# Kernel tuning notes

Measured on AMD Instinct MI355X. Metric: run time of the kernel, lower is better.

The kernel has to match this reference:

```python
import jax, jax.numpy as jnp
import numpy as np

EMB_DIM = 1024
HEAD_NUM = 16
HEAD_DIM = EMB_DIM // HEAD_NUM
B, S = 2, 2048


def setup_inputs() -> dict:
    key = jax.random.key(0)
    k_x, k_wqkv, k_bqkv, k_wo, k_bo = jax.random.split(key, 5)
    x = jax.random.normal(k_x, (B, S, EMB_DIM), dtype=jnp.float32)
    # nn.Linear default init scale ~ 1/sqrt(fan_in); exact distribution irrelevant for a reference
    lim = 1.0 / np.sqrt(EMB_DIM)
    W_qkv = jax.random.uniform(k_wqkv, (EMB_DIM, 3 * EMB_DIM), jnp.float32, -lim, lim)
    b_qkv = jax.random.uniform(k_bqkv, (3 * EMB_DIM,), jnp.float32, -lim, lim)
    W_o = jax.random.uniform(k_wo, (EMB_DIM, EMB_DIM), jnp.float32, -lim, lim)
    b_o = jax.random.uniform(k_bo, (EMB_DIM,), jnp.float32, -lim, lim)
    mask = jnp.tril(jnp.ones((S, S), dtype=bool))  # causal mask as in casual_mask(seq_len)
    return {"x": x, "W_qkv": W_qkv, "b_qkv": b_qkv, "W_o": W_o, "b_o": b_o, "mask": mask}


def reference(x, W_qkv, b_qkv, W_o, b_o, mask):
    b, s, e = x.shape
    qkv = x @ W_qkv + b_qkv                      # [b, s, 3e]
    q, k, v = qkv[..., :e], qkv[..., e:2 * e], qkv[..., 2 * e:]
    # [b, s, h, d] -> [b, h, s, d]
    q = q.reshape(b, s, HEAD_NUM, HEAD_DIM).transpose(0, 2, 1, 3)
    k = k.reshape(b, s, HEAD_NUM, HEAD_DIM).transpose(0, 2, 1, 3)
    v = v.reshape(b, s, HEAD_NUM, HEAD_DIM).transpose(0, 2, 1, 3)
    scores = jnp.einsum("bhqd,bhkd->bhqk", q, k) / jnp.sqrt(jnp.float32(HEAD_DIM))
    scores = jnp.where(mask, scores, -jnp.inf)   # masked_fill(~mask, -inf)
    probs = jax.nn.softmax(scores, axis=-1)      # dropout is identity in eval mode
    out = jnp.einsum("bhqk,bhkd->bhqd", probs, v)
    out = out.transpose(0, 2, 1, 3).reshape(b, s, e)
    return out @ W_o + b_o
```

## Files before the change

### kernel.cpp

```cpp
#include <hip/hip_runtime.h>


typedef __attribute__((ext_vector_type(8))) short short8;
typedef __attribute__((ext_vector_type(4))) short short4v;
typedef __attribute__((ext_vector_type(4))) float floatx4;

#define NB 2
#define SEQ 2048
#define EMB 1024
#define NH 16
#define HD 64
#define M_ROWS (NB * SEQ)
#define N_QKV (3 * EMB)
#define SLOT_B 8448

#define GLL(g, l) __builtin_amdgcn_global_load_lds( \
    (const __attribute__((address_space(1))) void*)(g), \
    (__attribute__((address_space(3))) void*)(l), 16, 0, 0)

#if defined(__HIP_DEVICE_COMPILE__)
#define MFMA16K16(A, B, C) __builtin_amdgcn_mfma_f32_16x16x16bf16_1k(A, B, C, 0, 0, 0)
#else
#define MFMA16K16(A, B, C) (C)
#endif

static __device__ __forceinline__ unsigned short f2bf(float f) {
    union { float f; unsigned int u; } v; v.f = f;
    unsigned int r = v.u + 0x7FFFu + ((v.u >> 16) & 1u);
    return (unsigned short)(r >> 16);
}
static __device__ __forceinline__ float bf2f(unsigned short h) {
    union { unsigned int u; float f; } v; v.u = ((unsigned int)h) << 16;
    return v.f;
}

__global__ void prep(const float* __restrict__ x,
                     const float* __restrict__ Wqkv, const float* __restrict__ Wo,
                     unsigned short* __restrict__ x_bf,
                     unsigned short* __restrict__ wqkvT, unsigned short* __restrict__ woT) {
    __shared__ unsigned short tile[32][33];
    int z = blockIdx.z;
    int tx = threadIdx.x, ty = threadIdx.y;
    if (z == 2) {
        int id = ((int)blockIdx.y * 96 + (int)blockIdx.x) * 256 + ty * 32 + tx;
        const int n4 = M_ROWS * EMB / 4;
        for (int i = id; i < n4; i += 96 * 32 * 256) {
            float4 v = ((const float4*)x)[i];
            unsigned long long p = (unsigned long long)f2bf(v.x)
                | ((unsigned long long)f2bf(v.y) << 16)
                | ((unsigned long long)f2bf(v.z) << 32)
                | ((unsigned long long)f2bf(v.w) << 48);
            ((unsigned long long*)x_bf)[i] = p;
        }
        return;
    }
    int C = z ? EMB : N_QKV;
    if ((int)blockIdx.x * 32 >= C) return;
    const float* in = z ? Wo : Wqkv;
    unsigned short* out = z ? woT : wqkvT;
    const int R = EMB;
    int c0 = blockIdx.x * 32, r0 = blockIdx.y * 32;
    #pragma unroll
    for (int j = 0; j < 4; ++j)
        tile[ty + j * 8][tx] = f2bf(in[(size_t)(r0 + ty + j * 8) * C + c0 + tx]);
    __syncthreads();
    #pragma unroll
    for (int j = 0; j < 4; ++j)
        out[(size_t)(c0 + ty + j * 8) * R + r0 + tx] = tile[tx][ty + j * 8];
}

#define CTS 130

__global__ __launch_bounds__(256) void qkv_gemm(
    const unsigned short* __restrict__ A,
    const unsigned short* __restrict__ Bt,
    const float* __restrict__ bias,
    unsigned short* __restrict__ qb, unsigned short* __restrict__ kb,
    unsigned short* __restrict__ vb)
{
    const int K = EMB;
    __shared__ __align__(16) unsigned short smem[128 * CTS];

    int t = threadIdx.x;
    int m0 = blockIdx.y * 128;
    int n0 = blockIdx.x * 128;
    int w = t >> 6, lane = t & 63, quad = lane >> 4, lcol = lane & 15;
    int wr = w >> 1, wc = w & 1;

    floatx4 zero = {0.f, 0.f, 0.f, 0.f};
    floatx4 acc[4][4];
    #pragma unroll
    for (int i = 0; i < 4; ++i)
        #pragma unroll
        for (int j = 0; j < 4; ++j) acc[i][j] = zero;

    const unsigned short* a0 = A  + (size_t)(m0 + (t >> 2)) * K + ((t & 3) << 3);
    const unsigned short* b0 = Bt + (size_t)(n0 + (t >> 2)) * K + ((t & 3) << 3);
    unsigned short* la = &smem[t << 3];

    GLL(a0, la);
    GLL(a0 + 64 * K, la + 2048);
    GLL(b0, la + 4096);
    GLL(b0 + 64 * K, la + 6144);

    for (int k0 = 0; k0 < K; k0 += 32) {
        int cur = (k0 >> 5) & 1, nxt = cur ^ 1;
        __syncthreads();
        if (k0 + 32 < K) {
            GLL(a0 + k0 + 32, la + nxt * 8192);
            GLL(a0 + 64 * K + k0 + 32, la + nxt * 8192 + 2048);
            GLL(b0 + k0 + 32, la + nxt * 8192 + 4096);
            GLL(b0 + 64 * K + k0 + 32, la + nxt * 8192 + 6144);
        }
        const unsigned short* As = &smem[cur * 8192];
        const unsigned short* Bs = As + 4096;
        short8 af[4], bfm[4];
        #pragma unroll
        for (int i = 0; i < 4; ++i)
            af[i] = *(const short8*)(&As[(wr * 64 + i * 16 + lcol) * 32 + quad * 8]);
        #pragma unroll
        for (int j = 0; j < 4; ++j)
            bfm[j] = *(const short8*)(&Bs[(wc * 64 + j * 16 + lcol) * 32 + quad * 8]);
        #pragma unroll
        for (int i = 0; i < 4; ++i)
            #pragma unroll
            for (int j = 0; j < 4; ++j)
                acc[i][j] = __builtin_amdgcn_mfma_f32_16x16x32_bf16(af[i], bfm[j], acc[i][j], 0, 0, 0);
    }

    bool isV = (n0 >= 2 * EMB);
    __syncthreads();
    #pragma unroll
    for (int i = 0; i < 4; ++i) {
        int row0 = wr * 64 + i * 16 + quad * 4;
        #pragma unroll
        for (int j = 0; j < 4; ++j) {
            int col = wc * 64 + j * 16 + lcol;
            float bv = bias[n0 + col];
            #pragma unroll
            for (int r = 0; r < 4; ++r) {
                unsigned short hv = f2bf(acc[i][j][r] + bv);
                if (isV) smem[col * CTS + row0 + r] = hv;
                else     smem[(row0 + r) * CTS + col] = hv;
            }
        }
    }
    __syncthreads();

    int b = m0 >> 11, s0 = m0 & 2047;
    int hbase = (n0 & 1023) >> 6;
    if (!isV) {
        unsigned short* dst = (n0 >= EMB) ? kb : qb;
        #pragma unroll
        for (int it = 0; it < 8; ++it) {
            int job = it * 32 + (t >> 3);
            int tok = job & 127, hh = job >> 7;
            int chunk = t & 7;
            short8 vv = *(const short8*)(&smem[tok * CTS + hh * 64 + chunk * 8]);
            size_t g = ((size_t)((b * NH + hbase + hh) * SEQ + s0 + tok)) * HD + chunk * 8;
            *(short8*)(&dst[g]) = vv;
        }
    } else {
        #pragma unroll
        for (int it = 0; it < 8; ++it) {
            int job = it * 32 + (t >> 3);
            int f = job & 127, half = job >> 7;
            int chunk = (t & 7) + half * 8;
            short8 vv = *(const short8*)(&smem[f * CTS + chunk * 8]);
            int h = hbase + (f >> 6), d = f & 63;
            size_t g = ((size_t)((b * NH + h) * HD + d)) * SEQ + s0 + chunk * 8;
            *(short8*)(&vb[g]) = vv;
        }
    }
}

__global__ __launch_bounds__(256) void attn_partial(
    const unsigned short* __restrict__ Q,
    const unsigned short* __restrict__ Kk,
    const unsigned short* __restrict__ Vt,
    unsigned short* __restrict__ Out,
    unsigned char* __restrict__ Part)
{
    __shared__ __align__(16) unsigned short Ks[2][64 * 64];
    __shared__ __align__(16) unsigned short Vs[2][64 * 64];

    int u = blockIdx.x;
    int bh = blockIdx.y;
    int qt, c;
    if (u < 16) { qt = u; c = 0; }
    else { int v = u - 16; qt = 16 + (v >> 1); c = v & 1; }
    int ktBeg = c << 4;
    int ktEnd = (c == 0 && qt >= 16) ? 16 : (qt + 1);

    int q0 = qt * 64;
    int t = threadIdx.x;
    int w = t >> 6, lane = t & 63, quad = lane >> 4, lcol = lane & 15;
    const size_t hoff = (size_t)bh * SEQ * HD;
    const float SC = 0.18033688011112043f;

    const unsigned short* qp = Q + hoff + (size_t)(q0 + 16 * w + lcol) * HD + quad * 8;
    short8 aq0 = *(const short8*)qp, aq1 = *(const short8*)(qp + 32);

    int srow = t >> 3;
    int ss   = (t & 7) ^ (srow & 7);
    const unsigned short* kgl = Kk + hoff + (size_t)srow * HD + ss * 8;
    const unsigned short* vgl = Vt + hoff + (size_t)srow * SEQ + ss * 8;
    unsigned short* kld = &Ks[0][t * 8];
    unsigned short* vld = &Vs[0][t * 8];

    floatx4 zero = {0.f, 0.f, 0.f, 0.f};
    floatx4 O[4];
    floatx4 lacc = zero;
    #pragma unroll
    for (int d = 0; d < 4; ++d) O[d] = zero;

    short4v ones4;
    #pragma unroll
    for (int j = 0; j < 4; ++j) ones4[j] = (short)0x3F80;

    {
        int k0 = ktBeg * 64;
        GLL(kgl + (size_t)k0 * HD, kld);
        GLL(kgl + (size_t)(k0 + 32) * HD, kld + 2048);
        GLL(vgl + k0, vld);
        GLL(vgl + (size_t)32 * SEQ + k0, vld + 2048);
    }

    int sx0 = (quad ^ (lcol & 7)) << 3;
    int sx1 = sx0 ^ 32;

    for (int kt = ktBeg; kt < ktEnd; ++kt) {
        int cur = kt & 1, nxt = cur ^ 1;
        __syncthreads();
        if (kt + 1 < ktEnd) {
            int k0 = (kt + 1) * 64;
            GLL(kgl + (size_t)k0 * HD, kld + nxt * 4096);
            GLL(kgl + (size_t)(k0 + 32) * HD, kld + nxt * 4096 + 2048);
            GLL(vgl + k0, vld + nxt * 4096);
            GLL(vgl + (size_t)32 * SEQ + k0, vld + nxt * 4096 + 2048);
        }

        const unsigned short* ksr = &Ks[cur][0];
        const unsigned short* vsr = &Vs[cur][0];
        short8 bk0[4], bk1[4];
        #pragma unroll
        for (int tc = 0; tc < 4; ++tc) {
            int rb = (tc * 16 + lcol) << 6;
            bk0[tc] = *(const short8*)(ksr + rb + sx0);
            bk1[tc] = *(const short8*)(ksr + rb + sx1);
        }

        floatx4 sacc[4];
        #pragma unroll
        for (int tc = 0; tc < 4; ++tc) {
            sacc[tc] = __builtin_amdgcn_mfma_f32_16x16x32_bf16(bk0[tc], aq0, zero, 0, 0, 0);
            sacc[tc] = __builtin_amdgcn_mfma_f32_16x16x32_bf16(bk1[tc], aq1, sacc[tc], 0, 0, 0);
        }

        short4v pk[4];
        if (kt == qt) {
            int qrow = q0 + 16 * w + lcol;
            int kbase = kt * 64 + quad * 4;
            #pragma unroll
            for (int tc = 0; tc < 4; ++tc) {
                #pragma unroll
                for (int r = 0; r < 4; ++r) {
                    float p = __builtin_amdgcn_exp2f(sacc[tc][r] * SC);
                    if (kbase + tc * 16 + r > qrow) p = 0.f;
                    pk[tc][r] = (short)f2bf(p);
                }
            }
        } else {
            #pragma unroll
            for (int tc = 0; tc < 4; ++tc) {
                #pragma unroll
                for (int r = 0; r < 4; ++r)
                    pk[tc][r] = (short)f2bf(__builtin_amdgcn_exp2f(sacc[tc][r] * SC));
            }
        }

        #pragma unroll
        for (int td = 0; td < 4; ++td) {
            short4v va[4];
            #pragma unroll
            for (int tc = 0; tc < 4; ++tc) {
                int seg = ((tc << 1) + (quad >> 1)) ^ (lcol & 7);
                va[tc] = *(const short4v*)(vsr + ((td * 16 + lcol) << 6) + (seg << 3) + ((quad & 1) << 2));
            }
            #pragma unroll
            for (int tc = 0; tc < 4; ++tc)
                O[td] = MFMA16K16(va[tc], pk[tc], O[td]);
        }
        #pragma unroll
        for (int tc = 0; tc < 4; ++tc)
            lacc = MFMA16K16(ones4, pk[tc], lacc);
    }

    int qrow = q0 + 16 * w + lcol;
    if (qt < 16) {
        int b = bh >> 4, h = bh & 15;
        float inv = 1.0f / lacc[0];
        size_t obase = ((size_t)b * SEQ + qrow) * EMB + (size_t)h * HD + quad * 4;
        #pragma unroll
        for (int td = 0; td < 4; ++td) {
            short4v ov;
            #pragma unroll
            for (int r = 0; r < 4; ++r) ov[r] = (short)f2bf(O[td][r] * inv);
            *(short4v*)(&Out[obase + td * 16]) = ov;
        }
    } else {
        unsigned char* sp = Part + ((size_t)(bh * 16 + (qt - 16)) * 2 + c) * SLOT_B;
        unsigned short* sO = (unsigned short*)sp;
        float* sL = (float*)(sp + 8192);
        int ql = 16 * w + lcol;
        #pragma unroll
        for (int td = 0; td < 4; ++td) {
            short4v ov;
            #pragma unroll
            for (int r = 0; r < 4; ++r) ov[r] = (short)f2bf(O[td][r]);
            *(short4v*)(&sO[ql * 64 + td * 16 + quad * 4]) = ov;
        }
        if (quad == 0) sL[ql] = lacc[0];
    }
}

__global__ __launch_bounds__(256) void attn_combine(
    const unsigned char* __restrict__ Part, unsigned short* __restrict__ Out)
{
    int qh = blockIdx.x;
    int bh = blockIdx.y;
    int qt = 16 + qh;
    const unsigned char* s0 = Part + ((size_t)(bh * 16 + qh) * 2) * SLOT_B;
    const unsigned char* s1 = s0 + SLOT_B;
    const unsigned short* O0 = (const unsigned short*)s0;
    const unsigned short* O1 = (const unsigned short*)s1;
    const float* L0 = (const float*)(s0 + 8192);
    const float* L1 = (const float*)(s1 + 8192);
    int b = bh >> 4, h = bh & 15;
    size_t obase = ((size_t)b * SEQ + qt * 64) * EMB + (size_t)h * HD;
    int t = threadIdx.x;
    #pragma unroll
    for (int it = 0; it < 16; ++it) {
        int idx = it * 256 + t;
        int row = idx >> 6, col = idx & 63;
        float lv = L0[row] + L1[row];
        float v = (bf2f(O0[idx]) + bf2f(O1[idx])) / lv;
        Out[obase + (size_t)row * EMB + col] = f2bf(v);
    }
}

__global__ __launch_bounds__(256) void oproj_gemm(
    const unsigned short* __restrict__ A,
    const unsigned short* __restrict__ Bt,
    const float* __restrict__ bias,
    float* __restrict__ Cout)
{
    const int K = EMB;
    __shared__ __align__(16) unsigned short smem[2 * 8192];
    int t = threadIdx.x;
    int m0 = blockIdx.y * 128;
    int n0 = blockIdx.x * 128;
    int w = t >> 6, lane = t & 63, quad = lane >> 4, lcol = lane & 15;
    int wr = w >> 1, wc = w & 1;

    floatx4 zero = {0.f, 0.f, 0.f, 0.f};
    floatx4 acc[4][4];
    #pragma unroll
    for (int i = 0; i < 4; ++i)
        #pragma unroll
        for (int j = 0; j < 4; ++j) acc[i][j] = zero;

    const unsigned short* a0 = A  + (size_t)(m0 + (t >> 2)) * K + ((t & 3) << 3);
    const unsigned short* b0 = Bt + (size_t)(n0 + (t >> 2)) * K + ((t & 3) << 3);
    unsigned short* la = &smem[t << 3];

    GLL(a0, la);
    GLL(a0 + 64 * K, la + 2048);
    GLL(b0, la + 4096);
    GLL(b0 + 64 * K, la + 6144);

    for (int k0 = 0; k0 < K; k0 += 32) {
        int cur = (k0 >> 5) & 1, nxt = cur ^ 1;
        __syncthreads();
        if (k0 + 32 < K) {
            GLL(a0 + k0 + 32, la + nxt * 8192);
            GLL(a0 + 64 * K + k0 + 32, la + nxt * 8192 + 2048);
            GLL(b0 + k0 + 32, la + nxt * 8192 + 4096);
            GLL(b0 + 64 * K + k0 + 32, la + nxt * 8192 + 6144);
        }
        const unsigned short* As = &smem[cur * 8192];
        const unsigned short* Bs = As + 4096;
        short8 af[4], bfm[4];
        #pragma unroll
        for (int i = 0; i < 4; ++i)
            af[i] = *(const short8*)(&As[(wr * 64 + i * 16 + lcol) * 32 + quad * 8]);
        #pragma unroll
        for (int j = 0; j < 4; ++j)
            bfm[j] = *(const short8*)(&Bs[(wc * 64 + j * 16 + lcol) * 32 + quad * 8]);
        #pragma unroll
        for (int i = 0; i < 4; ++i)
            #pragma unroll
            for (int j = 0; j < 4; ++j)
                acc[i][j] = __builtin_amdgcn_mfma_f32_16x16x32_bf16(af[i], bfm[j], acc[i][j], 0, 0, 0);
    }

    #pragma unroll
    for (int i = 0; i < 4; ++i) {
        int m = m0 + wr * 64 + i * 16 + quad * 4;
        #pragma unroll
        for (int j = 0; j < 4; ++j) {
            int n = n0 + wc * 64 + j * 16 + lcol;
            float bv = bias[n];
            #pragma unroll
            for (int r = 0; r < 4; ++r)
                Cout[(size_t)(m + r) * EMB + n] = acc[i][j][r] + bv;
        }
    }
}

extern "C" void kernel_launch(void* const* d_in, const int* in_sizes, int n_in,
                              void* d_out, int out_size, void* d_ws, size_t ws_size,
                              hipStream_t stream) {
    (void)in_sizes; (void)n_in; (void)out_size; (void)ws_size;
    char* ws = (char*)d_ws;
    const size_t OFF_X     = 0;
    const size_t OFF_WQKVT = OFF_X     + (size_t)M_ROWS * EMB * 2;
    const size_t OFF_WOT   = OFF_WQKVT + (size_t)N_QKV * EMB * 2;
    const size_t OFF_Q     = OFF_WOT   + (size_t)EMB * EMB * 2;
    const size_t OFF_K     = OFF_Q     + (size_t)M_ROWS * EMB * 2;
    const size_t OFF_V     = OFF_K     + (size_t)M_ROWS * EMB * 2;
    const size_t OFF_ATTN  = OFF_V     + (size_t)M_ROWS * EMB * 2;
    const size_t OFF_PART  = OFF_ATTN  + (size_t)M_ROWS * EMB * 2;

    const float* x    = (const float*)d_in[0];
    const float* Wqkv = (const float*)d_in[1];
    const float* bqkv = (const float*)d_in[2];
    const float* Wo   = (const float*)d_in[3];
    const float* bo   = (const float*)d_in[4];

    unsigned short* x_bf  = (unsigned short*)(ws + OFF_X);
    unsigned short* wqkvT = (unsigned short*)(ws + OFF_WQKVT);
    unsigned short* woT   = (unsigned short*)(ws + OFF_WOT);
    unsigned short* qb    = (unsigned short*)(ws + OFF_Q);
    unsigned short* kb    = (unsigned short*)(ws + OFF_K);
    unsigned short* vb    = (unsigned short*)(ws + OFF_V);
    unsigned short* attn  = (unsigned short*)(ws + OFF_ATTN);
    unsigned char*  part  = (unsigned char*)(ws + OFF_PART);

    prep<<<dim3(96, 32, 3), dim3(32, 8), 0, stream>>>(x, Wqkv, Wo, x_bf, wqkvT, woT);

    qkv_gemm<<<dim3(N_QKV / 128, M_ROWS / 128), 256, 0, stream>>>(x_bf, wqkvT, bqkv, qb, kb, vb);
    attn_partial<<<dim3(48, NB * NH), 256, 0, stream>>>(qb, kb, vb, attn, part);
    attn_combine<<<dim3(16, NB * NH), 256, 0, stream>>>(part, attn);
    oproj_gemm<<<dim3(EMB / 128, M_ROWS / 128), 256, 0, stream>>>(attn, woT, bo, (float*)d_out);
}
```

Baseline: 199.5 us.

## Fuse split-K attention combine into partial kernel via atomic last-arriver

The separate attn_combine launch is removed. The last of the two split blocks, detected by an atomic counter whose flags are zeroed in prep, now merges the partial outputs in place. The softmax scale is folded into Q in the QKV GEMM epilogue. V fragments are loaded before the MFMA loop, and bf16 packing uses a byte-permute truncation instead of round-to-nearest. This saves a kernel launch and some per-element multiplies, at the cost of threadfences and atomics, more register pressure, and slightly different rounding.

```diff
diff --git a/kernel.cpp b/kernel.cpp
--- a/kernel.cpp
+++ b/kernel.cpp
@@ -13,6 +13,7 @@
 #define M_ROWS (NB * SEQ)
 #define N_QKV (3 * EMB)
 #define SLOT_B 8448
+#define SC_Q 0.18033688011112043f
 
 #define GLL(g, l) __builtin_amdgcn_global_load_lds( \
     (const __attribute__((address_space(1))) void*)(g), \
@@ -33,11 +34,16 @@
     union { unsigned int u; float f; } v; v.u = ((unsigned int)h) << 16;
     return v.f;
 }
+static __device__ __forceinline__ unsigned int pkhi(float a, float b) {
+    union { float f; unsigned int u; } ua, ub; ua.f = a; ub.f = b;
+    return __builtin_amdgcn_perm(ub.u, ua.u, 0x07060302u);
+}
 
 __global__ void prep(const float* __restrict__ x,
                      const float* __restrict__ Wqkv, const float* __restrict__ Wo,
                      unsigned short* __restrict__ x_bf,
-                     unsigned short* __restrict__ wqkvT, unsigned short* __restrict__ woT) {
+                     unsigned short* __restrict__ wqkvT, unsigned short* __restrict__ woT,
+                     int* __restrict__ flags) {
     __shared__ unsigned short tile[32][33];
     int z = blockIdx.z;
     int tx = threadIdx.x, ty = threadIdx.y;
@@ -56,6 +62,11 @@
     }
     int C = z ? EMB : N_QKV;
     if ((int)blockIdx.x * 32 >= C) return;
+    if (z == 1 && blockIdx.x == 0 && blockIdx.y == 0) {
+        int id = ty * 32 + tx;
+        flags[id] = 0;
+        flags[id + 256] = 0;
+    }
     const float* in = z ? Wo : Wqkv;
     unsigned short* out = z ? woT : wqkvT;
     const int R = EMB;
@@ -129,6 +140,7 @@
     }
 
     bool isV = (n0 >= 2 * EMB);
+    float scl = (n0 < EMB) ? SC_Q : 1.0f;
     __syncthreads();
     #pragma unroll
     for (int i = 0; i < 4; ++i) {
@@ -139,7 +151,7 @@
             float bv = bias[n0 + col];
             #pragma unroll
             for (int r = 0; r < 4; ++r) {
-                unsigned short hv = f2bf(acc[i][j][r] + bv);
+                unsigned short hv = f2bf((acc[i][j][r] + bv) * scl);
                 if (isV) smem[col * CTS + row0 + r] = hv;
                 else     smem[(row0 + r) * CTS + col] = hv;
             }
@@ -179,10 +191,12 @@
     const unsigned short* __restrict__ Kk,
     const unsigned short* __restrict__ Vt,
     unsigned short* __restrict__ Out,
-    unsigned char* __restrict__ Part)
+    unsigned char* __restrict__ Part,
+    int* __restrict__ Flag)
 {
     __shared__ __align__(16) unsigned short Ks[2][64 * 64];
     __shared__ __align__(16) unsigned short Vs[2][64 * 64];
+    __shared__ int sArr;
 
     int u = blockIdx.x;
     int bh = blockIdx.y;
@@ -196,7 +210,6 @@
     int t = threadIdx.x;
     int w = t >> 6, lane = t & 63, quad = lane >> 4, lcol = lane & 15;
     const size_t hoff = (size_t)bh * SEQ * HD;
-    const float SC = 0.18033688011112043f;
 
     const unsigned short* qp = Q + hoff + (size_t)(q0 + 16 * w + lcol) * HD + quad * 8;
     short8 aq0 = *(const short8*)qp, aq1 = *(const short8*)(qp + 32);
@@ -228,6 +241,7 @@
 
     int sx0 = (quad ^ (lcol & 7)) << 3;
     int sx1 = sx0 ^ 32;
+    int qrow = q0 + 16 * w + lcol;
 
     for (int kt = ktBeg; kt < ktEnd; ++kt) {
         int cur = kt & 1, nxt = cur ^ 1;
@@ -249,6 +263,14 @@
             bk0[tc] = *(const short8*)(ksr + rb + sx0);
             bk1[tc] = *(const short8*)(ksr + rb + sx1);
         }
+        short4v vaf[4][4];
+        #pragma unroll
+        for (int td = 0; td < 4; ++td)
+            #pragma unroll
+            for (int tc = 0; tc < 4; ++tc) {
+                int seg = ((tc << 1) + (quad >> 1)) ^ (lcol & 7);
+                vaf[td][tc] = *(const short4v*)(vsr + ((td * 16 + lcol) << 6) + (seg << 3) + ((quad & 1) << 2));
+            }
 
         floatx4 sacc[4];
         #pragma unroll
@@ -257,95 +279,83 @@
             sacc[tc] = __builtin_amdgcn_mfma_f32_16x16x32_bf16(bk1[tc], aq1, sacc[tc], 0, 0, 0);
         }
 
+        bool diag = (kt == qt);
         short4v pk[4];
-        if (kt == qt) {
-            int qrow = q0 + 16 * w + lcol;
-            int kbase = kt * 64 + quad * 4;
-            #pragma unroll
-            for (int tc = 0; tc < 4; ++tc) {
-                #pragma unroll
-                for (int r = 0; r < 4; ++r) {
-                    float p = __builtin_amdgcn_exp2f(sacc[tc][r] * SC);
-                    if (kbase + tc * 16 + r > qrow) p = 0.f;
-                    pk[tc][r] = (short)f2bf(p);
-                }
-            }
-        } else {
-            #pragma unroll
-            for (int tc = 0; tc < 4; ++tc) {
+        #pragma unroll
+        for (int tc = 0; tc < 4; ++tc) {
+            float pv[4];
+            #pragma unroll
+            for (int r = 0; r < 4; ++r)
+                pv[r] = __builtin_amdgcn_exp2f(sacc[tc][r]);
+            if (diag) {
+                int kbase = kt * 64 + tc * 16 + quad * 4;
                 #pragma unroll
                 for (int r = 0; r < 4; ++r)
-                    pk[tc][r] = (short)f2bf(__builtin_amdgcn_exp2f(sacc[tc][r] * SC));
+                    if (kbase + r > qrow) pv[r] = 0.f;
             }
-        }
-
-        #pragma unroll
-        for (int td = 0; td < 4; ++td) {
-            short4v va[4];
-            #pragma unroll
-            for (int tc = 0; tc < 4; ++tc) {
-                int seg = ((tc << 1) + (quad >> 1)) ^ (lcol & 7);
-                va[tc] = *(const short4v*)(vsr + ((td * 16 + lcol) << 6) + (seg << 3) + ((quad & 1) << 2));
-            }
+            union { unsigned int u[2]; short4v s; } cv;
+            cv.u[0] = pkhi(pv[0], pv[1]);
+            cv.u[1] = pkhi(pv[2], pv[3]);
+            pk[tc] = cv.s;
+        }
+
+        #pragma unroll
+        for (int td = 0; td < 4; ++td)
             #pragma unroll
             for (int tc = 0; tc < 4; ++tc)
-                O[td] = MFMA16K16(va[tc], pk[tc], O[td]);
-        }
+                O[td] = MFMA16K16(vaf[td][tc], pk[tc], O[td]);
         #pragma unroll
         for (int tc = 0; tc < 4; ++tc)
             lacc = MFMA16K16(ones4, pk[tc], lacc);
     }
 
-    int qrow = q0 + 16 * w + lcol;
+    int b = bh >> 4, h = bh & 15;
     if (qt < 16) {
-        int b = bh >> 4, h = bh & 15;
         float inv = 1.0f / lacc[0];
         size_t obase = ((size_t)b * SEQ + qrow) * EMB + (size_t)h * HD + quad * 4;
         #pragma unroll
         for (int td = 0; td < 4; ++td) {
-            short4v ov;
-            #pragma unroll
-            for (int r = 0; r < 4; ++r) ov[r] = (short)f2bf(O[td][r] * inv);
-            *(short4v*)(&Out[obase + td * 16]) = ov;
+            union { unsigned int u[2]; short4v s; } cv;
+            cv.u[0] = pkhi(O[td][0] * inv, O[td][1] * inv);
+            cv.u[1] = pkhi(O[td][2] * inv, O[td][3] * inv);
+            *(short4v*)(&Out[obase + td * 16]) = cv.s;
         }
     } else {
-        unsigned char* sp = Part + ((size_t)(bh * 16 + (qt - 16)) * 2 + c) * SLOT_B;
+        int qh = qt - 16;
+        unsigned char* sp = Part + ((size_t)(bh * 16 + qh) * 2 + c) * SLOT_B;
         unsigned short* sO = (unsigned short*)sp;
         float* sL = (float*)(sp + 8192);
         int ql = 16 * w + lcol;
         #pragma unroll
         for (int td = 0; td < 4; ++td) {
-            short4v ov;
-            #pragma unroll
-            for (int r = 0; r < 4; ++r) ov[r] = (short)f2bf(O[td][r]);
-            *(short4v*)(&sO[ql * 64 + td * 16 + quad * 4]) = ov;
+            union { unsigned int u[2]; short4v s; } cv;
+            cv.u[0] = pkhi(O[td][0], O[td][1]);
+            cv.u[1] = pkhi(O[td][2], O[td][3]);
+            *(short4v*)(&sO[ql * 64 + td * 16 + quad * 4]) = cv.s;
         }
         if (quad == 0) sL[ql] = lacc[0];
-    }
-}
-
-__global__ __launch_bounds__(256) void attn_combine(
-    const unsigned char* __restrict__ Part, unsigned short* __restrict__ Out)
-{
-    int qh = blockIdx.x;
-    int bh = blockIdx.y;
-    int qt = 16 + qh;
-    const unsigned char* s0 = Part + ((size_t)(bh * 16 + qh) * 2) * SLOT_B;
-    const unsigned char* s1 = s0 + SLOT_B;
-    const unsigned short* O0 = (const unsigned short*)s0;
-    const unsigned short* O1 = (const unsigned short*)s1;
-    const float* L0 = (const float*)(s0 + 8192);
-    const float* L1 = (const float*)(s1 + 8192);
-    int b = bh >> 4, h = bh & 15;
-    size_t obase = ((size_t)b * SEQ + qt * 64) * EMB + (size_t)h * HD;
-    int t = threadIdx.x;
-    #pragma unroll
-    for (int it = 0; it < 16; ++it) {
-        int idx = it * 256 + t;
-        int row = idx >> 6, col = idx & 63;
-        float lv = L0[row] + L1[row];
-        float v = (bf2f(O0[idx]) + bf2f(O1[idx])) / lv;
-        Out[obase + (size_t)row * EMB + col] = f2bf(v);
+
+        __threadfence();
+        if (t == 0) sArr = atomicAdd(&Flag[bh * 16 + qh], 1);
+        __syncthreads();
+        if (sArr == 1) {
+            __threadfence();
+            const unsigned char* s0 = Part + ((size_t)(bh * 16 + qh) * 2) * SLOT_B;
+            const unsigned char* s1 = s0 + SLOT_B;
+            const unsigned short* O0 = (const unsigned short*)s0;
+            const unsigned short* O1 = (const unsigned short*)s1;
+            const float* L0 = (const float*)(s0 + 8192);
+            const float* L1 = (const float*)(s1 + 8192);
+            size_t obase = ((size_t)b * SEQ + qt * 64) * EMB + (size_t)h * HD;
+            #pragma unroll
+            for (int it = 0; it < 16; ++it) {
+                int idx = it * 256 + t;
+                int row = idx >> 6, col = idx & 63;
+                float lv = L0[row] + L1[row];
+                float v = (bf2f(O0[idx]) + bf2f(O1[idx])) / lv;
+                Out[obase + (size_t)row * EMB + col] = f2bf(v);
+            }
+        }
     }
 }
 
@@ -431,6 +441,7 @@
     const size_t OFF_V     = OFF_K     + (size_t)M_ROWS * EMB * 2;
     const size_t OFF_ATTN  = OFF_V     + (size_t)M_ROWS * EMB * 2;
     const size_t OFF_PART  = OFF_ATTN  + (size_t)M_ROWS * EMB * 2;
+    const size_t OFF_FLAG  = OFF_PART  + (size_t)32 * 16 * 2 * SLOT_B;
 
     const float* x    = (const float*)d_in[0];
     const float* Wqkv = (const float*)d_in[1];
@@ -446,11 +457,11 @@
     unsigned short* vb    = (unsigned short*)(ws + OFF_V);
     unsigned short* attn  = (unsigned short*)(ws + OFF_ATTN);
     unsigned char*  part  = (unsigned char*)(ws + OFF_PART);
-
-    prep<<<dim3(96, 32, 3), dim3(32, 8), 0, stream>>>(x, Wqkv, Wo, x_bf, wqkvT, woT);
+    int*            flags = (int*)(ws + OFF_FLAG);
+
+    prep<<<dim3(96, 32, 3), dim3(32, 8), 0, stream>>>(x, Wqkv, Wo, x_bf, wqkvT, woT, flags);
 
     qkv_gemm<<<dim3(N_QKV / 128, M_ROWS / 128), 256, 0, stream>>>(x_bf, wqkvT, bqkv, qb, kb, vb);
-    attn_partial<<<dim3(48, NB * NH), 256, 0, stream>>>(qb, kb, vb, attn, part);
-    attn_combine<<<dim3(16, NB * NH), 256, 0, stream>>>(part, attn);
+    attn_partial<<<dim3(48, NB * NH), 256, 0, stream>>>(qb, kb, vb, attn, part, flags);
     oproj_gemm<<<dim3(EMB / 128, M_ROWS / 128), 256, 0, stream>>>(attn, woT, bo, (float*)d_out);
 }
```

Measured after the change: 416.1 us. 109% more time.
